# Optimization experiments

Hardware: AMD Instinct MI355X
Metric: run time of the kernel (lower is better)

The kernel has to match this reference:

```python
import jax, jax.numpy as jnp
import numpy as np

PI = np.float32(np.pi)

def _normalize(x, eps=1e-6):
    # matches torch F.normalize: x / max(||x||, eps)
    return x / jnp.maximum(jnp.linalg.norm(x, axis=-1, keepdims=True), eps)

def _linear2srgb(x, eps=1e-8):
    lin = 12.92 * x
    exp = 1.055 * jnp.power(jnp.maximum(x, eps), 1.0 / 2.4) - 0.055
    return jnp.where(x <= 0.0031308, lin, exp)

def _ggx_specular(nrm, surf2c, surf2l, roughness, fresnel):
    # nrm [N,3], surf2c [N,3], surf2l [1,L,3] (unit), roughness [N,1], fresnel [N,3]
    L = _normalize(surf2l)                                  # [1,L,3]
    V = _normalize(surf2c)                                  # [N,3]
    H = _normalize((L + V[:, None, :]) / 2.0)               # [N,L,3]
    N = _normalize(nrm)                                     # [N,3]
    NoV = jnp.sum(V * N, axis=-1, keepdims=True)            # [N,1]
    N = N * jnp.sign(NoV)
    NoL = jnp.clip(jnp.sum(N[:, None, :] * L, axis=-1, keepdims=True), 1e-6, 1.0)  # [N,L,1]
    NoV = jnp.clip(jnp.sum(N * V, axis=-1, keepdims=True), 1e-6, 1.0)              # [N,1]
    NoH = jnp.clip(jnp.sum(N[:, None, :] * H, axis=-1, keepdims=True), 1e-6, 1.0)  # [N,L,1]
    VoH = jnp.clip(jnp.sum(V[:, None, :] * H, axis=-1, keepdims=True), 1e-6, 1.0)  # [N,L,1]
    alpha = roughness * roughness                            # [N,1]
    alpha2 = alpha * alpha
    k = (alpha + 2.0 * roughness + 1.0) / 8.0                # [N,1]
    FMi = ((-5.55473) * VoH - 6.98316) * VoH                 # [N,L,1]
    frac0 = fresnel[:, None, :] + (1.0 - fresnel[:, None, :]) * jnp.power(2.0, FMi)  # [N,L,3]
    frac = frac0 * alpha2[:, None, :]                        # [N,L,3]
    nom0 = NoH * NoH * (alpha2[:, None, :] - 1.0) + 1.0      # [N,L,1]
    nom1 = NoV[:, None, :] * (1.0 - k[:, None, :]) + k[:, None, :]  # [N,1,1]
    nom2 = NoL * (1.0 - k[:, None, :]) + k[:, None, :]       # [N,L,1]
    nom = jnp.clip(4.0 * PI * nom0 * nom0 * nom1 * nom2, 1e-6, 4.0 * PI)
    return frac / nom                                        # [N,L,3]

def setup_inputs() -> dict:
    key = jax.random.key(0)
    ks = jax.random.split(key, 9)
    N, L = 32768, 512
    f32 = jnp.float32
    return {
        'viewdirs': jax.random.normal(ks[0], (N, 3), f32),
        'albedo': jax.random.uniform(ks[1], (N, 3), dtype=f32),
        'roughness': jax.random.uniform(ks[2], (N, 1), dtype=f32),
        'fresnel': jnp.full((N, 3), 0.04, dtype=f32),
        'normal': jax.random.normal(ks[3], (N, 3), f32),
        'light_dirs': jax.random.normal(ks[4], (L, 3), f32),
        'light_area_weight': jax.random.uniform(ks[5], (L,), dtype=f32),
        'env_rgbs': jax.random.uniform(ks[6], (L, 3), dtype=f32),
        'visibility': jax.random.uniform(ks[7], (N, L, 1), dtype=f32),
        'indirect_light': jax.random.uniform(ks[8], (N, L, 3), dtype=f32),
    }

def reference(viewdirs, albedo, roughness, fresnel, normal, light_dirs,
              light_area_weight, env_rgbs, visibility, indirect_light):
    # sample(): albedo clamp, roughness affine+clamp, normal normalize
    albedo = jnp.clip(albedo, 0.0, 1.0)
    roughness = jnp.clip(roughness * 0.9 + 0.09, 0.0, 1.0)
    nrm = _normalize(normal)
    surf2l = _normalize(light_dirs)[None, :, :]              # [1,L,3]
    surf2c = _normalize(-viewdirs)                            # [N,3]
    cosine = jnp.clip(jnp.einsum('lk,nk->nl', _normalize(light_dirs), nrm), 0.0)  # [N,L]
    mask = (cosine > 1e-6)[..., None]                         # [N,L,1]
    vis = visibility * mask                                   # scatter-into-zeros equivalent
    ind = indirect_light * mask
    spec = _ggx_specular(nrm, surf2c, surf2l, roughness, fresnel)  # [N,L,3]
    brdf = albedo[:, None, :] / PI + spec                      # [N,L,3]
    direct = env_rgbs[None, :, :]                              # [1,L,3] (light_idx all zero)
    w = cosine[..., None] * light_area_weight[None, :, None]   # [N,L,1]
    light_rgbs = vis * direct + ind
    rgb = _linear2srgb(jnp.clip(jnp.sum(brdf * light_rgbs * w, axis=1), 0.0, 1.0))
    wo_indir = _linear2srgb(jnp.sum(brdf * (vis * direct) * w, axis=1))
    wo_vis = _linear2srgb(jnp.sum(brdf * direct * w, axis=1))
    indir = _linear2srgb(jnp.sum(brdf * ind * w, axis=1))
    return rgb, wo_indir, wo_vis, indir
```

## Files before the change

### kernel.cpp

```cpp
#include <hip/hip_runtime.h>
#include <math.h>


#define PI_F     3.14159265358979323846f
#define FOURPI_F (4.0f * PI_F)
#define MAXL     512

__device__ __forceinline__ float fast_rcp(float x)  { float r; asm("v_rcp_f32 %0, %1" : "=v"(r) : "v"(x)); return r; }
__device__ __forceinline__ float fast_rsq(float x)  { float r; asm("v_rsq_f32 %0, %1" : "=v"(r) : "v"(x)); return r; }
__device__ __forceinline__ float fast_exp2(float x) { float r; asm("v_exp_f32 %0, %1" : "=v"(r) : "v"(x)); return r; }
__device__ __forceinline__ float fast_log2(float x) { float r; asm("v_log_f32 %0, %1" : "=v"(r) : "v"(x)); return r; }

__device__ __forceinline__ float lin2srgb(float x) {
  float lin = 12.92f * x;
  float xe  = fmaxf(x, 1e-8f);
  float e   = 1.055f * fast_exp2(fast_log2(xe) * (1.0f / 2.4f)) - 0.055f;
  return (x <= 0.0031308f) ? lin : e;
}

__device__ __forceinline__ float clamp01(float x) { return fminf(fmaxf(x, 0.0f), 1.0f); }
__device__ __forceinline__ float clampe(float x)  { return fminf(fmaxf(x, 1e-6f), 1.0f); }

template <int LC>
__global__ void __launch_bounds__(256)
tensoir_render(const float* __restrict__ viewdirs,
               const float* __restrict__ albedo,
               const float* __restrict__ roughness,
               const float* __restrict__ fresnel,
               const float* __restrict__ normal,
               const float* __restrict__ light_dirs,
               const float* __restrict__ law,
               const float* __restrict__ env_rgbs,
               const float* __restrict__ visibility,
               const float* __restrict__ indirect,
               float* __restrict__ out,
               int N, int Lrt) {
  __shared__ float4 s_ld[MAXL];
  __shared__ float4 s_env[MAXL];

  const int L = LC ? LC : Lrt;
  const int tid = threadIdx.x;

  for (int l = tid; l < L && l < MAXL; l += 256) {
    float lx = light_dirs[3 * l + 0];
    float ly = light_dirs[3 * l + 1];
    float lz = light_dirs[3 * l + 2];
    float inv = fast_rsq(fmaxf(lx * lx + ly * ly + lz * lz, 1e-12f));
    s_ld[l]  = make_float4(lx * inv, ly * inv, lz * inv, law[l]);
    s_env[l] = make_float4(env_rgbs[3 * l + 0], env_rgbs[3 * l + 1],
                           env_rgbs[3 * l + 2], 0.0f);
  }
  __syncthreads();

  const int lane = tid & 63;
  const int n = blockIdx.x * 4 + (tid >> 6);
  if (n >= N) return;

  float vx = -viewdirs[3 * n + 0], vy = -viewdirs[3 * n + 1], vz = -viewdirs[3 * n + 2];
  {
    float inv = fast_rsq(fmaxf(vx * vx + vy * vy + vz * vz, 1e-12f));
    vx *= inv; vy *= inv; vz *= inv;
  }
  float nx = normal[3 * n + 0], ny = normal[3 * n + 1], nz = normal[3 * n + 2];
  {
    float inv = fast_rsq(fmaxf(nx * nx + ny * ny + nz * nz, 1e-12f));
    nx *= inv; ny *= inv; nz *= inv;
  }
  float rough = roughness[n];
  rough = clamp01(rough * 0.9f + 0.09f);
  const float alpha  = rough * rough;
  const float alpha2 = alpha * alpha;
  const float kk     = (alpha + 2.0f * rough + 1.0f) * 0.125f;
  const float onemk  = 1.0f - kk;

  const float fr = fresnel[3 * n + 0], fg = fresnel[3 * n + 1], fb = fresnel[3 * n + 2];
  const float omfr = 1.0f - fr, omfg = 1.0f - fg, omfb = 1.0f - fb;
  const float ar = clamp01(albedo[3 * n + 0]) * (1.0f / PI_F);
  const float ag = clamp01(albedo[3 * n + 1]) * (1.0f / PI_F);
  const float ab = clamp01(albedo[3 * n + 2]) * (1.0f / PI_F);

  const float NoV0 = vx * nx + vy * ny + vz * nz;
  const float sgn  = (NoV0 >= 0.0f) ? 1.0f : -1.0f;
  const float Nfx = nx * sgn, Nfy = ny * sgn, Nfz = nz * sgn;
  const float NoV  = clampe(fabsf(NoV0));
  const float nom1 = NoV * onemk + kk;

  float s1r = 0, s1g = 0, s1b = 0;
  float s2r = 0, s2g = 0, s2b = 0;
  float s3r = 0, s3g = 0, s3b = 0;

  const float* visrow = visibility + (size_t)n * L;
  const float* indrow = indirect + (size_t)n * L * 3;

  auto body = [&](int i) {
    const float4 ld = s_ld[i];
    const float4 ev = s_env[i];
    const float visv = visrow[i];
    const float ir = indrow[3 * i + 0];
    const float ig = indrow[3 * i + 1];
    const float ib = indrow[3 * i + 2];

    const float cosine = fmaxf(ld.x * nx + ld.y * ny + ld.z * nz, 0.0f);
    const bool  mask   = cosine > 1e-6f;
    const float w      = cosine * ld.w;

    const float hx = ld.x + vx, hy = ld.y + vy, hz = ld.z + vz;
    const float hinv = fast_rsq(fmaxf(hx * hx + hy * hy + hz * hz, 1e-12f));

    const float NoL = clampe(Nfx * ld.x + Nfy * ld.y + Nfz * ld.z);
    const float NoH = clampe((Nfx * hx + Nfy * hy + Nfz * hz) * hinv);
    const float VoH = clampe((vx * hx + vy * hy + vz * hz) * hinv);

    const float FMi = (-5.55473f * VoH - 6.98316f) * VoH;
    const float p2  = fast_exp2(FMi);
    const float nom0 = NoH * NoH * (alpha2 - 1.0f) + 1.0f;
    const float nom2 = NoL * onemk + kk;
    const float nom  = fminf(fmaxf(FOURPI_F * nom0 * nom0 * nom1 * nom2, 1e-6f), FOURPI_F);
    const float ss   = alpha2 * fast_rcp(nom);

    const float br = ar + (fr + omfr * p2) * ss;
    const float bg = ag + (fg + omfg * p2) * ss;
    const float bb = ab + (fb + omfb * p2) * ss;

    const float vism = mask ? visv : 0.0f;
    const float irm  = mask ? ir : 0.0f;
    const float igm  = mask ? ig : 0.0f;
    const float ibm  = mask ? ib : 0.0f;

    const float twr = br * w, twg = bg * w, twb = bb * w;

    s1r += twr * (vism * ev.x);  s1g += twg * (vism * ev.y);  s1b += twb * (vism * ev.z);
    s2r += twr * ev.x;           s2g += twg * ev.y;           s2b += twb * ev.z;
    s3r += twr * irm;            s3g += twg * igm;            s3b += twb * ibm;
  };

  if (LC) {
    constexpr int NITER = LC ? LC / 64 : 1;
#pragma unroll 4
    for (int j = 0; j < NITER; ++j) body(lane + 64 * j);
  } else {
    for (int i = lane; i < L; i += 64) body(i);
  }

#define WAVE_RED(v)                 \
  do {                              \
    v += __shfl_xor(v, 32);         \
    v += __shfl_xor(v, 16);         \
    v += __shfl_xor(v, 8);          \
    v += __shfl_xor(v, 4);          \
    v += __shfl_xor(v, 2);          \
    v += __shfl_xor(v, 1);          \
  } while (0)
  WAVE_RED(s1r); WAVE_RED(s1g); WAVE_RED(s1b);
  WAVE_RED(s2r); WAVE_RED(s2g); WAVE_RED(s2b);
  WAVE_RED(s3r); WAVE_RED(s3g); WAVE_RED(s3b);
#undef WAVE_RED

  if (lane == 0) {
    const size_t stride = (size_t)3 * N;
    float* o0 = out + 3 * (size_t)n;
    float* o1 = o0 + stride;
    float* o2 = o1 + stride;
    float* o3 = o2 + stride;
    o0[0] = lin2srgb(clamp01(s1r + s3r));
    o0[1] = lin2srgb(clamp01(s1g + s3g));
    o0[2] = lin2srgb(clamp01(s1b + s3b));
    o1[0] = lin2srgb(s1r); o1[1] = lin2srgb(s1g); o1[2] = lin2srgb(s1b);
    o2[0] = lin2srgb(s2r); o2[1] = lin2srgb(s2g); o2[2] = lin2srgb(s2b);
    o3[0] = lin2srgb(s3r); o3[1] = lin2srgb(s3g); o3[2] = lin2srgb(s3b);
  }
}

extern "C" void kernel_launch(void* const* d_in, const int* in_sizes, int n_in,
                              void* d_out, int out_size, void* d_ws, size_t ws_size,
                              hipStream_t stream) {
  const float* viewdirs   = (const float*)d_in[0];
  const float* albedo     = (const float*)d_in[1];
  const float* roughness  = (const float*)d_in[2];
  const float* fresnel    = (const float*)d_in[3];
  const float* normal     = (const float*)d_in[4];
  const float* light_dirs = (const float*)d_in[5];
  const float* law        = (const float*)d_in[6];
  const float* env_rgbs   = (const float*)d_in[7];
  const float* visibility = (const float*)d_in[8];
  const float* indirect   = (const float*)d_in[9];
  float* out = (float*)d_out;

  const int N = in_sizes[0] / 3;
  const int L = in_sizes[6];

  dim3 block(256);
  dim3 grid((N + 3) / 4);

  if (L == 512) {
    hipLaunchKernelGGL(tensoir_render<512>, grid, block, 0, stream,
                       viewdirs, albedo, roughness, fresnel, normal,
                       light_dirs, law, env_rgbs, visibility, indirect,
                       out, N, L);
  } else {
    hipLaunchKernelGGL(tensoir_render<0>, grid, block, 0, stream,
                       viewdirs, albedo, roughness, fresnel, normal,
                       light_dirs, law, env_rgbs, visibility, indirect,
                       out, N, L);
  }
}
```

Before: 54.71 us.

## Vectorize per-point visibility/indirect loads as float4 with lane-contiguous light groups

Each lane now handles four consecutive lights per group, so visibility and indirect rows are read with float4 loads (one vis float4 and three indirect float4s per group) instead of strided scalar loads. Shared-memory light data is reindexed into four interleaved banks so the matching directions and env colors line up with those quads. Per-point input loads are moved before the barrier to overlap with the shared-memory fill, and out-of-range points are clamped instead of returning early. The cost is higher register pressure from issuing all eight vector loads up front and full unrolling of eight light bodies.

```diff
diff --git a/kernel.cpp b/kernel.cpp
--- a/kernel.cpp
+++ b/kernel.cpp
@@ -5,6 +5,7 @@
 #define PI_F     3.14159265358979323846f
 #define FOURPI_F (4.0f * PI_F)
 #define MAXL     512
+#define MAXQ     (MAXL / 4)
 
 __device__ __forceinline__ float fast_rcp(float x)  { float r; asm("v_rcp_f32 %0, %1" : "=v"(r) : "v"(x)); return r; }
 __device__ __forceinline__ float fast_rsq(float x)  { float r; asm("v_rsq_f32 %0, %1" : "=v"(r) : "v"(x)); return r; }
@@ -35,49 +36,51 @@
                const float* __restrict__ indirect,
                float* __restrict__ out,
                int N, int Lrt) {
-  __shared__ float4 s_ld[MAXL];
-  __shared__ float4 s_env[MAXL];
+  __shared__ float4 s_dirw[4][MAXQ];
+  __shared__ float4 s_env [4][MAXQ];
 
   const int L = LC ? LC : Lrt;
   const int tid = threadIdx.x;
+  const int lane = tid & 63;
+  int n = blockIdx.x * 4 + (tid >> 6);
+  if (n >= N) n = N - 1;
+
+  float vx = -viewdirs[3 * n + 0], vy = -viewdirs[3 * n + 1], vz = -viewdirs[3 * n + 2];
+  float nx = normal[3 * n + 0], ny = normal[3 * n + 1], nz = normal[3 * n + 2];
+  float rough0 = roughness[n];
+  const float fr = fresnel[3 * n + 0], fg = fresnel[3 * n + 1], fb = fresnel[3 * n + 2];
+  float ar0 = albedo[3 * n + 0], ag0 = albedo[3 * n + 1], ab0 = albedo[3 * n + 2];
 
   for (int l = tid; l < L && l < MAXL; l += 256) {
     float lx = light_dirs[3 * l + 0];
     float ly = light_dirs[3 * l + 1];
     float lz = light_dirs[3 * l + 2];
     float inv = fast_rsq(fmaxf(lx * lx + ly * ly + lz * lz, 1e-12f));
-    s_ld[l]  = make_float4(lx * inv, ly * inv, lz * inv, law[l]);
-    s_env[l] = make_float4(env_rgbs[3 * l + 0], env_rgbs[3 * l + 1],
-                           env_rgbs[3 * l + 2], 0.0f);
+    s_dirw[l & 3][l >> 2] = make_float4(lx * inv, ly * inv, lz * inv, law[l]);
+    s_env [l & 3][l >> 2] = make_float4(env_rgbs[3 * l + 0], env_rgbs[3 * l + 1],
+                                        env_rgbs[3 * l + 2], 0.0f);
   }
   __syncthreads();
 
-  const int lane = tid & 63;
-  const int n = blockIdx.x * 4 + (tid >> 6);
-  if (n >= N) return;
-
-  float vx = -viewdirs[3 * n + 0], vy = -viewdirs[3 * n + 1], vz = -viewdirs[3 * n + 2];
   {
     float inv = fast_rsq(fmaxf(vx * vx + vy * vy + vz * vz, 1e-12f));
     vx *= inv; vy *= inv; vz *= inv;
   }
-  float nx = normal[3 * n + 0], ny = normal[3 * n + 1], nz = normal[3 * n + 2];
   {
     float inv = fast_rsq(fmaxf(nx * nx + ny * ny + nz * nz, 1e-12f));
     nx *= inv; ny *= inv; nz *= inv;
   }
-  float rough = roughness[n];
-  rough = clamp01(rough * 0.9f + 0.09f);
+  const float rough  = clamp01(rough0 * 0.9f + 0.09f);
   const float alpha  = rough * rough;
   const float alpha2 = alpha * alpha;
+  const float a2m1   = alpha2 - 1.0f;
   const float kk     = (alpha + 2.0f * rough + 1.0f) * 0.125f;
   const float onemk  = 1.0f - kk;
 
-  const float fr = fresnel[3 * n + 0], fg = fresnel[3 * n + 1], fb = fresnel[3 * n + 2];
   const float omfr = 1.0f - fr, omfg = 1.0f - fg, omfb = 1.0f - fb;
-  const float ar = clamp01(albedo[3 * n + 0]) * (1.0f / PI_F);
-  const float ag = clamp01(albedo[3 * n + 1]) * (1.0f / PI_F);
-  const float ab = clamp01(albedo[3 * n + 2]) * (1.0f / PI_F);
+  const float ar = clamp01(ar0) * (1.0f / PI_F);
+  const float ag = clamp01(ag0) * (1.0f / PI_F);
+  const float ab = clamp01(ab0) * (1.0f / PI_F);
 
   const float NoV0 = vx * nx + vy * ny + vz * nz;
   const float sgn  = (NoV0 >= 0.0f) ? 1.0f : -1.0f;
@@ -92,55 +95,84 @@
   const float* visrow = visibility + (size_t)n * L;
   const float* indrow = indirect + (size_t)n * L * 3;
 
-  auto body = [&](int i) {
-    const float4 ld = s_ld[i];
-    const float4 ev = s_env[i];
-    const float visv = visrow[i];
-    const float ir = indrow[3 * i + 0];
-    const float ig = indrow[3 * i + 1];
-    const float ib = indrow[3 * i + 2];
-
-    const float cosine = fmaxf(ld.x * nx + ld.y * ny + ld.z * nz, 0.0f);
-    const bool  mask   = cosine > 1e-6f;
-    const float w      = cosine * ld.w;
-
-    const float hx = ld.x + vx, hy = ld.y + vy, hz = ld.z + vz;
-    const float hinv = fast_rsq(fmaxf(hx * hx + hy * hy + hz * hz, 1e-12f));
-
-    const float NoL = clampe(Nfx * ld.x + Nfy * ld.y + Nfz * ld.z);
-    const float NoH = clampe((Nfx * hx + Nfy * hy + Nfz * hz) * hinv);
-    const float VoH = clampe((vx * hx + vy * hy + vz * hz) * hinv);
-
-    const float FMi = (-5.55473f * VoH - 6.98316f) * VoH;
-    const float p2  = fast_exp2(FMi);
-    const float nom0 = NoH * NoH * (alpha2 - 1.0f) + 1.0f;
-    const float nom2 = NoL * onemk + kk;
-    const float nom  = fminf(fmaxf(FOURPI_F * nom0 * nom0 * nom1 * nom2, 1e-6f), FOURPI_F);
-    const float ss   = alpha2 * fast_rcp(nom);
-
-    const float br = ar + (fr + omfr * p2) * ss;
-    const float bg = ag + (fg + omfg * p2) * ss;
-    const float bb = ab + (fb + omfb * p2) * ss;
-
-    const float vism = mask ? visv : 0.0f;
-    const float irm  = mask ? ir : 0.0f;
-    const float igm  = mask ? ig : 0.0f;
-    const float ibm  = mask ? ib : 0.0f;
-
-    const float twr = br * w, twg = bg * w, twb = bb * w;
-
-    s1r += twr * (vism * ev.x);  s1g += twg * (vism * ev.y);  s1b += twb * (vism * ev.z);
-    s2r += twr * ev.x;           s2g += twg * ev.y;           s2b += twb * ev.z;
-    s3r += twr * irm;            s3g += twg * igm;            s3b += twb * ibm;
-  };
-
-  if (LC) {
-    constexpr int NITER = LC ? LC / 64 : 1;
-#pragma unroll 4
-    for (int j = 0; j < NITER; ++j) body(lane + 64 * j);
+#define LIGHT_BODY(dw, ev, visv, ir_, ig_, ib_)                                 \
+  do {                                                                          \
+    const float cosine = fmaxf((dw).x * nx + (dw).y * ny + (dw).z * nz, 0.0f);  \
+    const bool  mask   = cosine > 1e-6f;                                        \
+    const float w      = cosine * (dw).w;                                       \
+    const float hx = (dw).x + vx, hy = (dw).y + vy, hz = (dw).z + vz;           \
+    const float hinv = fast_rsq(fmaxf(hx * hx + hy * hy + hz * hz, 1e-12f));    \
+    const float NoL = clampe(Nfx * (dw).x + Nfy * (dw).y + Nfz * (dw).z);       \
+    const float NoH = clampe((Nfx * hx + Nfy * hy + Nfz * hz) * hinv);          \
+    const float VoH = clampe((vx * hx + vy * hy + vz * hz) * hinv);             \
+    const float FMi = (-5.55473f * VoH - 6.98316f) * VoH;                       \
+    const float p2  = fast_exp2(FMi);                                           \
+    const float nom0 = NoH * NoH * a2m1 + 1.0f;                                 \
+    const float nom2 = NoL * onemk + kk;                                        \
+    const float nom  = fminf(fmaxf(FOURPI_F * nom0 * nom0 * nom1 * nom2, 1e-6f),\
+                             FOURPI_F);                                         \
+    const float ss   = alpha2 * fast_rcp(nom);                                  \
+    const float br = ar + (fr + omfr * p2) * ss;                                \
+    const float bg = ag + (fg + omfg * p2) * ss;                                \
+    const float bb = ab + (fb + omfb * p2) * ss;                                \
+    const float vism = mask ? (visv) : 0.0f;                                    \
+    const float irm  = mask ? (ir_) : 0.0f;                                     \
+    const float igm  = mask ? (ig_) : 0.0f;                                     \
+    const float ibm  = mask ? (ib_) : 0.0f;                                     \
+    const float twr = br * w, twg = bg * w, twb = bb * w;                       \
+    s1r += twr * (vism * (ev).x); s1g += twg * (vism * (ev).y);                 \
+    s1b += twb * (vism * (ev).z);                                               \
+    s2r += twr * (ev).x; s2g += twg * (ev).y; s2b += twb * (ev).z;              \
+    s3r += twr * irm;    s3g += twg * igm;    s3b += twb * ibm;                 \
+  } while (0)
+
+  if (LC == 512) {
+    const float4* vis4 = (const float4*)visrow;
+    const float4* ind4 = (const float4*)indrow;
+    const int q0 = lane;
+    const int q1 = lane + 64;
+
+    const float4 va = vis4[q0];
+    const float4 vb = vis4[q1];
+    const float4 ia0 = ind4[3 * q0 + 0];
+    const float4 ia1 = ind4[3 * q0 + 1];
+    const float4 ia2 = ind4[3 * q0 + 2];
+    const float4 ib0 = ind4[3 * q1 + 0];
+    const float4 ib1 = ind4[3 * q1 + 1];
+    const float4 ib2 = ind4[3 * q1 + 2];
+
+    {
+      const float4 d0 = s_dirw[0][q0], e0 = s_env[0][q0];
+      const float4 d1 = s_dirw[1][q0], e1 = s_env[1][q0];
+      const float4 d2 = s_dirw[2][q0], e2 = s_env[2][q0];
+      const float4 d3 = s_dirw[3][q0], e3 = s_env[3][q0];
+      LIGHT_BODY(d0, e0, va.x, ia0.x, ia0.y, ia0.z);
+      LIGHT_BODY(d1, e1, va.y, ia0.w, ia1.x, ia1.y);
+      LIGHT_BODY(d2, e2, va.z, ia1.z, ia1.w, ia2.x);
+      LIGHT_BODY(d3, e3, va.w, ia2.y, ia2.z, ia2.w);
+    }
+    {
+      const float4 d0 = s_dirw[0][q1], e0 = s_env[0][q1];
+      const float4 d1 = s_dirw[1][q1], e1 = s_env[1][q1];
+      const float4 d2 = s_dirw[2][q1], e2 = s_env[2][q1];
+      const float4 d3 = s_dirw[3][q1], e3 = s_env[3][q1];
+      LIGHT_BODY(d0, e0, vb.x, ib0.x, ib0.y, ib0.z);
+      LIGHT_BODY(d1, e1, vb.y, ib0.w, ib1.x, ib1.y);
+      LIGHT_BODY(d2, e2, vb.z, ib1.z, ib1.w, ib2.x);
+      LIGHT_BODY(d3, e3, vb.w, ib2.y, ib2.z, ib2.w);
+    }
   } else {
-    for (int i = lane; i < L; i += 64) body(i);
-  }
+    for (int i = lane; i < L; i += 64) {
+      const float4 dw = s_dirw[i & 3][i >> 2];
+      const float4 ev = s_env [i & 3][i >> 2];
+      const float visv = visrow[i];
+      const float ir = indrow[3 * i + 0];
+      const float ig = indrow[3 * i + 1];
+      const float ib = indrow[3 * i + 2];
+      LIGHT_BODY(dw, ev, visv, ir, ig, ib);
+    }
+  }
+#undef LIGHT_BODY
 
 #define WAVE_RED(v)                 \
   do {                              \
```

Result: slower. 61.48 us (+12.4%).
